# Performance work log

Hardware: AMD Instinct MI355X
Metric: run time of the kernel (lower is better)

## Reference

```python
import jax, jax.numpy as jnp
import numpy as np

B, N, K = 2, 8192, 16
D_IN, D_OUT = 32, 128
EPS = 1e-5


def _bn(x, gamma, beta):
    # x: (B, C, L); BatchNorm1d training-mode stats over (B, L)
    mean = x.mean(axis=(0, 2), keepdims=True)
    var = x.var(axis=(0, 2), keepdims=True)
    return gamma[None, :, None] * (x - mean) * jax.lax.rsqrt(var + EPS) + beta[None, :, None]


def _shared_mlp(x, w, b, gamma, beta, act):
    # SharedMLP: 1x1 Conv1d (channel GEMM) + BN + activation. x: (B, Cin, L)
    y = jnp.einsum('oi,bil->bol', w, x) + b[None, :, None]
    return act(_bn(y, gamma, beta))


def _attentive_pool(x, w, b):
    # x: (B, C, N, K); per-(b,n,k) Linear over C, softmax over K, weighted sum over K
    scores = jnp.einsum('oc,bcnk->bonk', w, x) + b[None, :, None, None]
    scores = jax.nn.softmax(scores, axis=-1)
    return jnp.sum(scores * x, axis=-1)  # (B, C, N)  (torch keeps K=1 dim; squeezed by SharedMLP reshape)


def _knn(coords, k):
    # brute-force squared-L2 KNN excluding self (faiss IndexFlatL2 semantics)
    sq = jnp.sum(coords * coords, axis=-1)  # (B, N)
    d2 = sq[:, :, None] + sq[:, None, :] - 2.0 * jnp.einsum('bid,bjd->bij', coords, coords)
    n = coords.shape[1]
    d2 = jnp.where(jnp.eye(n, dtype=bool)[None], jnp.inf, d2)
    neg, idx = jax.lax.top_k(-d2, k)  # ascending squared distance
    return idx, jnp.maximum(-neg, 0.0)


def _lse(coords, features, idx, dist, w, b, gamma, beta):
    # LocalSpatialEncoding: gather neighbor coords, build 10-ch relative features, MLP, concat
    Bq, Nq, Kq = idx.shape
    neighbor = jax.vmap(lambda c, i: c[i])(coords, idx)  # (B, N, K, 3)
    center = jnp.broadcast_to(coords[:, :, None, :], neighbor.shape)
    rel = center - neighbor
    spatial = jnp.concatenate([center, neighbor, rel, dist[..., None]], axis=-1)  # (B, N, K, 10)
    spatial = spatial.transpose(0, 3, 1, 2).reshape(Bq, 10, Nq * Kq)
    sf = _shared_mlp(spatial, w, b, gamma, beta, jax.nn.relu).reshape(Bq, -1, Nq, Kq)
    feat = jnp.broadcast_to(features[..., None], (Bq, features.shape[1], Nq, Kq))
    return jnp.concatenate([sf, feat], axis=1)


def _forward(coords, features,
             mlp1_w, mlp1_b, mlp1_g, mlp1_bt,
             lse1_w, lse1_b, lse1_g, lse1_bt,
             mlpp1_w, mlpp1_b, mlpp1_g, mlpp1_bt,
             lse2_w, lse2_b, lse2_g, lse2_bt,
             mlp2_w, mlp2_b, mlp2_g, mlp2_bt,
             res_w, res_b, res_g, res_bt,
             pool1_w, pool1_b, pool2_w, pool2_b):
    # faiss output is detached in torch (numpy round-trip) -> stop_gradient
    idx, dist = _knn(jax.lax.stop_gradient(coords), K)
    lrelu02 = lambda v: jnp.where(v >= 0, v, 0.2 * v)   # LeakyReLU(0.2)
    lrelu01 = lambda v: jnp.where(v >= 0, v, 0.01 * v)  # default LeakyReLU
    x = _shared_mlp(features, mlp1_w, mlp1_b, mlp1_g, mlp1_bt, lrelu02)      # (B, 64, N)
    x = _lse(coords, x, idx, dist, lse1_w, lse1_b, lse1_g, lse1_bt)          # (B, 128, N, K)
    x = _attentive_pool(x, pool1_w, pool1_b)                                  # (B, 128, N)
    x = _shared_mlp(x, mlpp1_w, mlpp1_b, mlpp1_g, mlpp1_bt, jax.nn.relu)     # (B, 32, N)
    x = _lse(coords, x, idx, dist, lse2_w, lse2_b, lse2_g, lse2_bt)          # (B, 64, N, K)
    x = _attentive_pool(x, pool2_w, pool2_b)                                  # (B, 64, N)
    x_main = _shared_mlp(x, mlp2_w, mlp2_b, mlp2_g, mlp2_bt, jax.nn.relu)    # (B, 128, N)
    resid = _shared_mlp(features, res_w, res_b, res_g, res_bt, jax.nn.relu)  # (B, 128, N)
    return lrelu01(jnp.concatenate([x_main, resid], axis=1))                 # (B, 256, N)


def setup_inputs() -> dict:
    key = jax.random.key(0)
    ks = iter(jax.random.split(key, 64))

    def lin(ci, co):
        w = jax.random.normal(next(ks), (co, ci), jnp.float32) / np.float32(np.sqrt(ci))
        b = jax.random.normal(next(ks), (co,), jnp.float32) * 0.01
        return w, b

    inp = {}
    inp['coords'] = jax.random.normal(next(ks), (B, N, 3), jnp.float32)
    inp['features'] = jax.random.normal(next(ks), (B, D_IN, N), jnp.float32)
    for name, ci, co in [('mlp1', D_IN, D_OUT // 2), ('lse1', 10, D_OUT // 2),
                         ('mlpp1', D_OUT, D_OUT // 4), ('lse2', 10, D_OUT // 4),
                         ('mlp2', D_OUT // 2, D_OUT), ('res', D_IN, D_OUT)]:
        w, b = lin(ci, co)
        inp[name + '_w'], inp[name + '_b'] = w, b
        inp[name + '_g'] = jnp.ones((co,), jnp.float32)
        inp[name + '_bt'] = jnp.zeros((co,), jnp.float32)
    for name, c in [('pool1', D_OUT), ('pool2', D_OUT // 2)]:
        w, b = lin(c, c)
        inp[name + '_w'], inp[name + '_b'] = w, b
    return inp


def reference(coords, features,
              mlp1_w, mlp1_b, mlp1_g, mlp1_bt,
              lse1_w, lse1_b, lse1_g, lse1_bt,
              mlpp1_w, mlpp1_b, mlpp1_g, mlpp1_bt,
              lse2_w, lse2_b, lse2_g, lse2_bt,
              mlp2_w, mlp2_b, mlp2_g, mlp2_bt,
              res_w, res_b, res_g, res_bt,
              pool1_w, pool1_b, pool2_w, pool2_b):
    return _forward(coords, features,
                    mlp1_w, mlp1_b, mlp1_g, mlp1_bt,
                    lse1_w, lse1_b, lse1_g, lse1_bt,
                    mlpp1_w, mlpp1_b, mlpp1_g, mlpp1_bt,
                    lse2_w, lse2_b, lse2_g, lse2_bt,
                    mlp2_w, mlp2_b, mlp2_g, mlp2_bt,
                    res_w, res_b, res_g, res_bt,
                    pool1_w, pool1_b, pool2_w, pool2_b)
```

## Files before the change

kernel.cpp:

```cpp
#include <hip/hip_runtime.h>

static constexpr int N_ = 8192;
static constexpr int B_ = 2;
static constexpr int K_ = 16;

typedef __attribute__((ext_vector_type(8))) short bf16x8;
typedef __attribute__((ext_vector_type(4))) float f32x4;

__device__ __forceinline__ short f2bf(float f) {
  unsigned int u = __float_as_uint(f);
  unsigned int r = (u + 0x7FFFu + ((u >> 16) & 1u)) >> 16;
  return (short)r;
}
__device__ __forceinline__ float bf2f(short h) {
  return __uint_as_float(((unsigned int)(unsigned short)h) << 16);
}

__global__ __launch_bounds__(512) void knn_kernel(const float* __restrict__ coords,
                                                  const int tbeg, const int tend,
                                                  float* __restrict__ skd, int* __restrict__ ski,
                                                  int* __restrict__ oidx, float* __restrict__ odist) {
  __shared__ float4 pts[2048];
  const int b = blockIdx.y;
  const int wv = threadIdx.x >> 6;
  const int lane = threadIdx.x & 63;
  const int q = blockIdx.x * 8 + wv;
  const float* cb = coords + (size_t)b * N_ * 3;
  const float qx = cb[q * 3 + 0], qy = cb[q * 3 + 1], qz = cb[q * 3 + 2];
  const float qsq = fmaf(qx, qx, fmaf(qy, qy, qz * qz));
  const int qblk = q & ~63;
  const unsigned long long qbit = ~(1ull << (q & 63));
  float kd = INFINITY;
  int ki = 0;
  if (tbeg > 0 && lane < 16) {
    kd = skd[((size_t)b * N_ + q) * K_ + lane];
    ki = ski[((size_t)b * N_ + q) * K_ + lane];
  }
  float tau = __shfl(kd, 15);
  for (int t0 = tbeg; t0 < tend; t0 += 2048) {
    __syncthreads();
    for (int i = threadIdx.x; i < 2048; i += 512) {
      const int p = t0 + i;
      const float x = cb[p * 3 + 0], y = cb[p * 3 + 1], z = cb[p * 3 + 2];
      pts[i] = make_float4(x, y, z, fmaf(x, x, fmaf(y, y, z * z)));
    }
    __syncthreads();
    for (int s = 0; s < 2048; s += 64) {
      const float4 p = pts[s + lane];
      const int base = t0 + s;
      const float dot = fmaf(qx, p.x, fmaf(qy, p.y, qz * p.z));
      const float d2 = fmaf(-2.0f, dot, qsq + p.w);
      unsigned long long m = __ballot(d2 < tau);
      if (base == qblk) m &= qbit;
      while (m) {
        const int src = __builtin_ctzll(m);
        const float dc = __shfl(d2, src);
        const int jc = base + src;
        const float sd = __shfl_up(kd, 1);
        const int si = __shfl_up(ki, 1);
        const bool c1 = kd > dc;
        const bool c2 = (lane > 0) && (sd > dc);
        kd = c1 ? (c2 ? sd : dc) : kd;
        ki = c1 ? (c2 ? si : jc) : ki;
        m &= (m - 1);
        tau = __shfl(kd, 15);
        m &= __ballot(d2 < tau);
      }
    }
  }
  if (lane < 16) {
    if (tend < N_) {
      skd[((size_t)b * N_ + q) * K_ + lane] = kd;
      ski[((size_t)b * N_ + q) * K_ + lane] = ki;
    } else {
      oidx[((size_t)b * N_ + q) * K_ + lane] = ki;
      odist[((size_t)b * N_ + q) * K_ + lane] = fmaxf(kd, 0.0f);
    }
  }
}

__device__ __forceinline__ float snn_get(const float* SNN, int a, int b) {
  const int i = a < b ? a : b, j = a < b ? b : a;
  return SNN[i == 0 ? j : (i == 1 ? 2 + j : 3 + j)];
}
__device__ __forceinline__ float mom_mean(int i, const float* C, const float* SN, float Sd) {
  if (i < 3) return 16.0f * C[i];
  if (i < 6) return SN[i - 3];
  if (i < 9) return 16.0f * C[i - 6] - SN[i - 6];
  return Sd;
}
__device__ __forceinline__ float mom_prod(int i, int j, const float* C, const float* SN,
                                          const float* SNN, float Sd, float Sdd, const float* SND) {
  const int ti = i < 3 ? 0 : (i < 6 ? 1 : (i < 9 ? 2 : 3));
  const int tj = j < 3 ? 0 : (j < 6 ? 1 : (j < 9 ? 2 : 3));
  const int a = (ti == 3) ? 0 : (i - ti * 3);
  const int bb = (tj == 3) ? 0 : (j - tj * 3);
  if (ti == 0 && tj == 0) return 16.0f * C[a] * C[bb];
  if (ti == 0 && tj == 1) return C[a] * SN[bb];
  if (ti == 0 && tj == 2) return C[a] * (16.0f * C[bb] - SN[bb]);
  if (ti == 0 && tj == 3) return C[a] * Sd;
  if (ti == 1 && tj == 1) return snn_get(SNN, a, bb);
  if (ti == 1 && tj == 2) return C[bb] * SN[a] - snn_get(SNN, a, bb);
  if (ti == 1 && tj == 3) return SND[a];
  if (ti == 2 && tj == 2) return 16.0f * C[a] * C[bb] - C[a] * SN[bb] - C[bb] * SN[a] + snn_get(SNN, a, bb);
  if (ti == 2 && tj == 3) return C[a] * Sd - SND[a];
  return Sdd;
}

__global__ __launch_bounds__(256) void moments_kernel(const float* __restrict__ coords,
                                                      const int* __restrict__ knn_i,
                                                      const float* __restrict__ knn_d,
                                                      double* __restrict__ mom) {
  __shared__ float sh[16][65];
  const int k = threadIdx.x & 15;
  const int pl = threadIdx.x >> 4;
  float accv = 0.0f;
  for (int batch = 0; batch < 4; ++batch) {
    const int pt = (blockIdx.x * 4 + batch) * 16 + pl;
    const int b = pt >> 13, n = pt & (N_ - 1);
    const float* cb = coords + (size_t)b * N_ * 3;
    const float cx = cb[n * 3 + 0], cy = cb[n * 3 + 1], cz = cb[n * 3 + 2];
    const int id = knn_i[(size_t)pt * K_ + k];
    const float dd = knn_d[(size_t)pt * K_ + k];
    const float nx = cb[id * 3 + 0], ny = cb[id * 3 + 1], nz = cb[id * 3 + 2];
    float v[14] = {nx, ny, nz, nx * nx, nx * ny, nx * nz, ny * ny, ny * nz, nz * nz,
                   dd, dd * dd, nx * dd, ny * dd, nz * dd};
#pragma unroll
    for (int e = 0; e < 14; ++e) {
      v[e] += __shfl_xor(v[e], 1);
      v[e] += __shfl_xor(v[e], 2);
      v[e] += __shfl_xor(v[e], 4);
      v[e] += __shfl_xor(v[e], 8);
    }
    if (k == 0) {
      const float C[3] = {cx, cy, cz};
      const float SN[3] = {v[0], v[1], v[2]};
      const float SNN[6] = {v[3], v[4], v[5], v[6], v[7], v[8]};
      const float Sd = v[9], Sdd = v[10];
      const float SND[3] = {v[11], v[12], v[13]};
      float m65[65];
      int e = 0;
#pragma unroll
      for (int i = 0; i < 10; ++i) m65[e++] = mom_mean(i, C, SN, Sd);
#pragma unroll
      for (int i = 0; i < 10; ++i)
#pragma unroll
        for (int j = i; j < 10; ++j) m65[e++] = mom_prod(i, j, C, SN, SNN, Sd, Sdd, SND);
#pragma unroll
      for (int q2 = 0; q2 < 65; ++q2) sh[pl][q2] = m65[q2];
    }
    __syncthreads();
    if (threadIdx.x < 65) {
      float s = 0.0f;
#pragma unroll
      for (int r = 0; r < 16; ++r) s += sh[r][threadIdx.x];
      accv += s;
    }
    __syncthreads();
  }
  if (threadIdx.x < 65) atomicAdd(&mom[threadIdx.x], (double)accv);
}

template <int CI, int CO>
__device__ __forceinline__ void conv_frag_seg(const float* __restrict__ w, short* __restrict__ H,
                                              short* __restrict__ L, int tid, int nthr) {
  constexpr int NT = CO / 16;
  for (int i = tid; i < CI * CO; i += nthr) {
    const int j = i & 7, l = (i >> 3) & 63, tmp = i >> 9;
    const int tt = tmp % NT, cc = tmp / NT;
    const int c = cc * 32 + (l >> 4) * 8 + j;
    const int o = tt * 16 + (l & 15);
    const float v = w[o * CI + c];
    const short h = f2bf(v);
    H[i] = h;
    L[i] = f2bf(v - bf2f(h));
  }
}

__global__ __launch_bounds__(256) void convert_kernel(
    const float* __restrict__ pw1, const float* __restrict__ pw2,
    short* __restrict__ wB1, short* __restrict__ wB2,
    const float* __restrict__ wm1, short* __restrict__ f1H, short* __restrict__ f1L,
    const float* __restrict__ wmp, short* __restrict__ f2H, short* __restrict__ f2L,
    const float* __restrict__ wm2, short* __restrict__ f3H, short* __restrict__ f3L,
    const float* __restrict__ wrs, short* __restrict__ fRH, short* __restrict__ fRL) {
  const int blk = blockIdx.x;
  if (blk < 8) {
    const int tid = blk * 256 + threadIdx.x;
    for (int i = tid; i < 128 * 128; i += 2048) wB1[i] = f2bf(pw1[i]);
  } else if (blk < 10) {
    const int tid = (blk - 8) * 256 + threadIdx.x;
    for (int i = tid; i < 64 * 64; i += 512) wB2[i] = f2bf(pw2[i]);
  } else if (blk < 12) {
    conv_frag_seg<32, 64>(wm1, f1H, f1L, (blk - 10) * 256 + threadIdx.x, 512);
  } else if (blk < 16) {
    conv_frag_seg<128, 32>(wmp, f2H, f2L, (blk - 12) * 256 + threadIdx.x, 1024);
  } else if (blk < 24) {
    conv_frag_seg<64, 128>(wm2, f3H, f3L, (blk - 16) * 256 + threadIdx.x, 2048);
  } else {
    conv_frag_seg<32, 128>(wrs, fRH, fRL, (blk - 24) * 256 + threadIdx.x, 1024);
  }
}

__global__ void setup_kernel(const double* __restrict__ mom,
                             const float* __restrict__ w1, const float* __restrict__ b1,
                             const float* __restrict__ g1, const float* __restrict__ t1,
                             const float* __restrict__ w2, const float* __restrict__ b2,
                             const float* __restrict__ g2, const float* __restrict__ t2,
                             float* __restrict__ w1f8, float* __restrict__ w2f8) {
  const int t = threadIdx.x;
  __shared__ double mu[10];
  __shared__ double S[10][10];
  const double cnt = (double)B_ * N_ * K_;
  if (t < 10) mu[t] = mom[t] / cnt;
  if (t < 55) {
    int e = t, i = 0;
    while (e >= 10 - i) { e -= 10 - i; ++i; }
    const int j = i + e;
    const double v = mom[10 + t] / cnt;
    S[i][j] = v;
    S[j][i] = v;
  }
  __syncthreads();
  const float *w, *bias, *gg, *bt;
  float *wf;
  int c;
  if (t < 64) { w = w1; bias = b1; gg = g1; bt = t1; wf = w1f8; c = t; }
  else if (t < 96) { w = w2; bias = b2; gg = g2; bt = t2; wf = w2f8; c = t - 64; }
  else return;
  double wd[10];
#pragma unroll
  for (int d = 0; d < 10; ++d) wd[d] = (double)w[c * 10 + d];
  const double cbv = (double)bias[c];
  double mz = cbv;
  for (int d = 0; d < 10; ++d) mz += wd[d] * mu[d];
  double e2 = cbv * cbv;
  for (int d = 0; d < 10; ++d) e2 += 2.0 * cbv * wd[d] * mu[d];
  for (int d = 0; d < 10; ++d)
    for (int e = 0; e < 10; ++e) e2 += wd[d] * wd[e] * S[d][e];
  const double var = e2 - mz * mz;
  const double a = (double)gg[c] / sqrt(var + 1e-5);
  const double shift = (double)bt[c] - a * mz;
  wf[c * 8 + 0] = (float)(a * (wd[0] + wd[6]));
  wf[c * 8 + 1] = (float)(a * (wd[1] + wd[7]));
  wf[c * 8 + 2] = (float)(a * (wd[2] + wd[8]));
  wf[c * 8 + 3] = (float)(a * (wd[3] - wd[6]));
  wf[c * 8 + 4] = (float)(a * (wd[4] - wd[7]));
  wf[c * 8 + 5] = (float)(a * (wd[5] - wd[8]));
  wf[c * 8 + 6] = (float)(a * wd[9]);
  wf[c * 8 + 7] = (float)(a * cbv + shift);
}

template <int CI, int CO, bool ROWMAJ>
__global__ __launch_bounds__(256) void gemm_mfma_kernel(const float* __restrict__ in,
                                                        const short* __restrict__ fragH,
                                                        const short* __restrict__ fragL,
                                                        const float* __restrict__ bias,
                                                        float* __restrict__ out,
                                                        double* __restrict__ sacc) {
  constexpr int NT = CO / 16;
  constexpr int NC = CI / 32;
  __shared__ float part[4][CO][2];
  const int wv = threadIdx.x >> 6, l = threadIdx.x & 63;
  const int col = l & 15, quad = l >> 4;
  const int p0 = blockIdx.x * 64 + wv * 16;
  const int pt = p0 + col;
  f32x4 d[NT];
#pragma unroll
  for (int t = 0; t < NT; ++t) {
    const float bv = bias[t * 16 + col];
    d[t][0] = bv; d[t][1] = bv; d[t][2] = bv; d[t][3] = bv;
  }
#pragma unroll
  for (int cc = 0; cc < NC; ++cc) {
    float xv[8];
    if (ROWMAJ) {
      const float* ip = in + (size_t)pt * CI + cc * 32 + quad * 8;
      *(float4*)&xv[0] = *(const float4*)ip;
      *(float4*)&xv[4] = *(const float4*)(ip + 4);
    } else {
      const int b = pt >> 13, n = pt & (N_ - 1);
      const float* ip = in + ((size_t)b * CI + cc * 32 + quad * 8) * N_ + n;
#pragma unroll
      for (int j = 0; j < 8; ++j) xv[j] = ip[(size_t)j * N_];
    }
    union { bf16x8 v; short u[8]; } AH, AL;
#pragma unroll
    for (int j = 0; j < 8; ++j) {
      const short h = f2bf(xv[j]);
      AH.u[j] = h;
      AL.u[j] = f2bf(xv[j] - bf2f(h));
    }
#pragma unroll
    for (int t = 0; t < NT; ++t) {
      const size_t fo = ((size_t)(cc * NT + t) * 64 + l) * 8;
      const bf16x8 BH = *(const bf16x8*)(fragH + fo);
      const bf16x8 BL = *(const bf16x8*)(fragL + fo);
      d[t] = __builtin_amdgcn_mfma_f32_16x16x32_bf16(AH.v, BH, d[t], 0, 0, 0);
      d[t] = __builtin_amdgcn_mfma_f32_16x16x32_bf16(AH.v, BL, d[t], 0, 0, 0);
      d[t] = __builtin_amdgcn_mfma_f32_16x16x32_bf16(AL.v, BH, d[t], 0, 0, 0);
    }
  }
#pragma unroll
  for (int t = 0; t < NT; ++t) {
#pragma unroll
    for (int r = 0; r < 4; ++r)
      out[(size_t)(p0 + quad * 4 + r) * CO + t * 16 + col] = d[t][r];
    float s1 = d[t][0] + d[t][1] + d[t][2] + d[t][3];
    float s2 = d[t][0] * d[t][0] + d[t][1] * d[t][1] + d[t][2] * d[t][2] + d[t][3] * d[t][3];
    s1 += __shfl_xor(s1, 16); s1 += __shfl_xor(s1, 32);
    s2 += __shfl_xor(s2, 16); s2 += __shfl_xor(s2, 32);
    if (quad == 0) { part[wv][t * 16 + col][0] = s1; part[wv][t * 16 + col][1] = s2; }
  }
  __syncthreads();
  if (threadIdx.x < CO) {
    const int o = threadIdx.x;
    atomicAdd(&sacc[o], (double)(part[0][o][0] + part[1][o][0] + part[2][o][0] + part[3][o][0]));
    atomicAdd(&sacc[CO + o], (double)(part[0][o][1] + part[1][o][1] + part[2][o][1] + part[3][o][1]));
  }
}

template <int CSF, int CF>
__global__ __launch_bounds__(256) void pool_kernel(
    const float* __restrict__ coords, const int* __restrict__ knn_i, const float* __restrict__ knn_d,
    const float* __restrict__ w8,
    const float* __restrict__ feat, const double* __restrict__ sfe,
    const float* __restrict__ gfe, const float* __restrict__ tfe,
    const float slope,
    const short* __restrict__ wB, const float* __restrict__ pb,
    float* __restrict__ out) {
  constexpr int C = CSF + CF;
  constexpr int CP = C + 4;
  constexpr int NT = C / 16;
  constexpr int NC = C / 32;
  __shared__ float xcat[4][16][CP];
  __shared__ float4 sp4[4][16];
  __shared__ float4 spc[4];
  const int g = threadIdx.x >> 6;
  const int l = threadIdx.x & 63;
  const int quad = l >> 4, col = l & 15;
  const int pid = blockIdx.x * 4 + g;
  const int b = pid >> 13, n = pid & (N_ - 1);
  const float* cb = coords + (size_t)b * N_ * 3;

  if (l < 16) {
    const int id = knn_i[(size_t)pid * K_ + l];
    const float dd = knn_d[(size_t)pid * K_ + l];
    const float nx = cb[id * 3 + 0], ny = cb[id * 3 + 1], nz = cb[id * 3 + 2];
    sp4[g][l] = make_float4(nx, ny, nz, dd);
    if (l == 0) spc[g] = make_float4(cb[n * 3 + 0], cb[n * 3 + 1], cb[n * 3 + 2], 0.0f);
  }
  if (l < CF) {
    const double cnt = (double)(B_ * N_);
    const double mean = sfe[l] / cnt;
    const double var = sfe[CF + l] / cnt - mean * mean;
    const double av = (double)gfe[l] / sqrt(var + 1e-5);
    const float af = (float)av;
    const float bfv = (float)((double)tfe[l] - av * mean);
    float v = feat[(size_t)pid * CF + l];
    v = af * v + bfv;
    v = (v >= 0.0f) ? v : slope * v;
#pragma unroll
    for (int j = 0; j < 16; ++j) xcat[g][j][CSF + l] = v;
  }
  __syncthreads();
  if (l < CSF) {
    const float4 wA = *(const float4*)(w8 + l * 8);
    const float4 wBv = *(const float4*)(w8 + l * 8 + 4);
    const float4 C4 = spc[g];
    const float tterm = wBv.w + wA.x * C4.x + wA.y * C4.y + wA.z * C4.z;
#pragma unroll
    for (int k = 0; k < 16; ++k) {
      const float4 nk = sp4[g][k];
      const float z = tterm + wA.w * nk.x + wBv.x * nk.y + wBv.y * nk.z + wBv.z * nk.w;
      xcat[g][k][l] = fmaxf(z, 0.0f);
    }
  }
  __syncthreads();
  f32x4 d[NT];
#pragma unroll
  for (int t = 0; t < NT; ++t) {
    const float pbv = pb[t * 16 + col];
    d[t][0] = pbv; d[t][1] = pbv; d[t][2] = pbv; d[t][3] = pbv;
  }
#pragma unroll
  for (int cc = 0; cc < NC; ++cc) {
    const float* xr = &xcat[g][col][cc * 32 + quad * 8];
    const float4 xa = *(const float4*)xr;
    const float4 xb = *(const float4*)(xr + 4);
    union { bf16x8 v; short u[8]; } A;
    A.u[0] = f2bf(xa.x); A.u[1] = f2bf(xa.y); A.u[2] = f2bf(xa.z); A.u[3] = f2bf(xa.w);
    A.u[4] = f2bf(xb.x); A.u[5] = f2bf(xb.y); A.u[6] = f2bf(xb.z); A.u[7] = f2bf(xb.w);
#pragma unroll
    for (int t = 0; t < NT; ++t) {
      const bf16x8 Bv = *(const bf16x8*)(wB + (size_t)(t * 16 + col) * C + cc * 32 + quad * 8);
      d[t] = __builtin_amdgcn_mfma_f32_16x16x32_bf16(A.v, Bv, d[t], 0, 0, 0);
    }
  }
#pragma unroll
  for (int t = 0; t < NT; ++t) {
    float mx = fmaxf(fmaxf(d[t][0], d[t][1]), fmaxf(d[t][2], d[t][3]));
    mx = fmaxf(mx, __shfl_xor(mx, 16));
    mx = fmaxf(mx, __shfl_xor(mx, 32));
    float e0 = __expf(d[t][0] - mx), e1 = __expf(d[t][1] - mx);
    float e2 = __expf(d[t][2] - mx), e3 = __expf(d[t][3] - mx);
    float s = e0 + e1 + e2 + e3;
    s += __shfl_xor(s, 16);
    s += __shfl_xor(s, 32);
    const int o = t * 16 + col;
    float part = e0 * xcat[g][quad * 4 + 0][o] + e1 * xcat[g][quad * 4 + 1][o] +
                 e2 * xcat[g][quad * 4 + 2][o] + e3 * xcat[g][quad * 4 + 3][o];
    part += __shfl_xor(part, 16);
    part += __shfl_xor(part, 32);
    if (quad == 0) out[(size_t)pid * C + o] = part / s;
  }
}

__global__ __launch_bounds__(256) void final_kernel(const float* __restrict__ y3,
                                                    const float* __restrict__ yr,
                                                    const double* __restrict__ s3,
                                                    const float* __restrict__ g3, const float* __restrict__ t3,
                                                    const double* __restrict__ sr,
                                                    const float* __restrict__ gr, const float* __restrict__ tr,
                                                    float* __restrict__ out) {
  __shared__ float tile[256 * 17];
  const int blk = blockIdx.x;
  const int b = blk >> 9;
  const int n0 = (blk & 511) << 4;
  const int c = threadIdx.x;
  const float* src;
  const double* sa;
  const float *gp, *tp;
  int cc;
  if (c < 128) { src = y3; sa = s3; gp = g3; tp = t3; cc = c; }
  else { src = yr; sa = sr; gp = gr; tp = tr; cc = c - 128; }
  const double cnt = (double)(B_ * N_);
  const double mean = sa[cc] / cnt;
  const double var = sa[128 + cc] / cnt - mean * mean;
  const double avd = (double)gp[cc] / sqrt(var + 1e-5);
  const float av = (float)avd;
  const float bv = (float)((double)tp[cc] - avd * mean);
#pragma unroll
  for (int nl = 0; nl < 16; ++nl) {
    const float x = av * src[((size_t)(b * N_ + n0 + nl)) * 128 + cc] + bv;
    tile[c * 17 + nl] = fmaxf(x, 0.0f);
  }
  __syncthreads();
  const int np = c & 15, grp = c >> 4;
#pragma unroll
  for (int j = 0; j < 16; ++j) {
    const int c2 = grp * 16 + j;
    out[((size_t)(b * 256 + c2)) * N_ + n0 + np] = tile[c2 * 17 + np];
  }
}

extern "C" void kernel_launch(void* const* d_in, const int* in_sizes, int n_in,
                              void* d_out, int out_size, void* d_ws, size_t ws_size,
                              hipStream_t stream) {
  (void)in_sizes; (void)n_in; (void)out_size; (void)ws_size;
  const float* coords   = (const float*)d_in[0];
  const float* features = (const float*)d_in[1];
  const float* mlp1_w = (const float*)d_in[2];
  const float* mlp1_b = (const float*)d_in[3];
  const float* mlp1_g = (const float*)d_in[4];
  const float* mlp1_t = (const float*)d_in[5];
  const float* lse1_w = (const float*)d_in[6];
  const float* lse1_b = (const float*)d_in[7];
  const float* lse1_g = (const float*)d_in[8];
  const float* lse1_t = (const float*)d_in[9];
  const float* mlpp1_w = (const float*)d_in[10];
  const float* mlpp1_b = (const float*)d_in[11];
  const float* mlpp1_g = (const float*)d_in[12];
  const float* mlpp1_t = (const float*)d_in[13];
  const float* lse2_w = (const float*)d_in[14];
  const float* lse2_b = (const float*)d_in[15];
  const float* lse2_g = (const float*)d_in[16];
  const float* lse2_t = (const float*)d_in[17];
  const float* mlp2_w = (const float*)d_in[18];
  const float* mlp2_b = (const float*)d_in[19];
  const float* mlp2_g = (const float*)d_in[20];
  const float* mlp2_t = (const float*)d_in[21];
  const float* res_w = (const float*)d_in[22];
  const float* res_b = (const float*)d_in[23];
  const float* res_g = (const float*)d_in[24];
  const float* res_t = (const float*)d_in[25];
  const float* pool1_w = (const float*)d_in[26];
  const float* pool1_b = (const float*)d_in[27];
  const float* pool2_w = (const float*)d_in[28];
  const float* pool2_b = (const float*)d_in[29];

  float* wsf = (float*)d_ws;
  int* knn_i = (int*)d_ws;
  float* knn_d = wsf + 262144;
  float* y1 = wsf + 524288;
  float* pooled1 = wsf + 1572864;
  float* y2 = wsf + 3670016;
  float* pooled2 = wsf + 4194304;
  float* y3 = wsf + 5242880;
  float* yr = wsf + 7340032;
  double* dacc = (double*)(wsf + 9437184);
  double* mom = dacc;
  double* sacc_mlp1 = dacc + 65;
  double* sacc_mlpp1 = dacc + 193;
  double* sacc_mlp2 = dacc + 257;
  double* sacc_res = dacc + 513;
  float* fpar = wsf + 9437184 + 1600;
  float* w1f8 = fpar;
  float* w2f8 = w1f8 + 512;
  short* wB1 = (short*)(w2f8 + 256);
  short* wB2 = wB1 + 16384;
  short* f1H = wB2 + 4096;
  short* f1L = f1H + 2048;
  short* f2H = f1L + 2048;
  short* f2L = f2H + 4096;
  short* f3H = f2L + 4096;
  short* f3L = f3H + 8192;
  short* fRH = f3L + 8192;
  short* fRL = fRH + 4096;
  float* skd = wsf + 9468224;
  int* ski = (int*)(skd + 262144);

  hipMemsetAsync(dacc, 0, 769 * sizeof(double), stream);
  knn_kernel<<<dim3(N_ / 8, B_), 512, 0, stream>>>(coords, 0, N_ / 2, skd, ski, knn_i, knn_d);
  knn_kernel<<<dim3(N_ / 8, B_), 512, 0, stream>>>(coords, N_ / 2, N_, skd, ski, knn_i, knn_d);
  convert_kernel<<<28, 256, 0, stream>>>(pool1_w, pool2_w, wB1, wB2,
                                         mlp1_w, f1H, f1L, mlpp1_w, f2H, f2L,
                                         mlp2_w, f3H, f3L, res_w, fRH, fRL);
  moments_kernel<<<256, 256, 0, stream>>>(coords, knn_i, knn_d, mom);
  setup_kernel<<<1, 128, 0, stream>>>(mom, lse1_w, lse1_b, lse1_g, lse1_t,
                                      lse2_w, lse2_b, lse2_g, lse2_t, w1f8, w2f8);
  gemm_mfma_kernel<32, 64, false><<<256, 256, 0, stream>>>(features, f1H, f1L, mlp1_b, y1, sacc_mlp1);
  pool_kernel<64, 64><<<B_ * N_ / 4, 256, 0, stream>>>(
      coords, knn_i, knn_d, w1f8, y1, sacc_mlp1, mlp1_g, mlp1_t, 0.2f, wB1, pool1_b, pooled1);
  gemm_mfma_kernel<128, 32, true><<<256, 256, 0, stream>>>(pooled1, f2H, f2L, mlpp1_b, y2, sacc_mlpp1);
  pool_kernel<32, 32><<<B_ * N_ / 4, 256, 0, stream>>>(
      coords, knn_i, knn_d, w2f8, y2, sacc_mlpp1, mlpp1_g, mlpp1_t, 0.0f, wB2, pool2_b, pooled2);
  gemm_mfma_kernel<64, 128, true><<<256, 256, 0, stream>>>(pooled2, f3H, f3L, mlp2_b, y3, sacc_mlp2);
  gemm_mfma_kernel<32, 128, false><<<256, 256, 0, stream>>>(features, fRH, fRL, res_b, yr, sacc_res);
  final_kernel<<<B_ * 512, 256, 0, stream>>>(y3, yr, sacc_mlp2, mlp2_g, mlp2_t,
                                             sacc_res, res_g, res_t, (float*)d_out);
}
```

Before: 414.9 us.

## Merge KNN passes and fuse prep, moments, setup and first GEMMs into fewer launches

The two-pass KNN (split target range with a scratch buffer carrying state between passes) becomes a single pass over all points, so the scratch round trip and one launch go away. The weight-conversion and moments kernels are merged into one prep_kernel. The setup kernel, the mlp1 GEMM and the residual GEMM are merged into one gemmA_kernel that picks its role from the block index. This cuts launch count and lets independent work share the GPU, but each KNN block now runs longer and the split may have been balancing occupancy.

```diff
diff --git a/kernel.cpp b/kernel.cpp
--- a/kernel.cpp
+++ b/kernel.cpp
@@ -17,9 +17,8 @@
 }
 
 __global__ __launch_bounds__(512) void knn_kernel(const float* __restrict__ coords,
-                                                  const int tbeg, const int tend,
-                                                  float* __restrict__ skd, int* __restrict__ ski,
-                                                  int* __restrict__ oidx, float* __restrict__ odist) {
+                                                  int* __restrict__ oidx,
+                                                  float* __restrict__ odist) {
   __shared__ float4 pts[2048];
   const int b = blockIdx.y;
   const int wv = threadIdx.x >> 6;
@@ -32,12 +31,8 @@
   const unsigned long long qbit = ~(1ull << (q & 63));
   float kd = INFINITY;
   int ki = 0;
-  if (tbeg > 0 && lane < 16) {
-    kd = skd[((size_t)b * N_ + q) * K_ + lane];
-    ki = ski[((size_t)b * N_ + q) * K_ + lane];
-  }
-  float tau = __shfl(kd, 15);
-  for (int t0 = tbeg; t0 < tend; t0 += 2048) {
+  float tau = INFINITY;
+  for (int t0 = 0; t0 < N_; t0 += 2048) {
     __syncthreads();
     for (int i = threadIdx.x; i < 2048; i += 512) {
       const int p = t0 + i;
@@ -69,13 +64,8 @@
     }
   }
   if (lane < 16) {
-    if (tend < N_) {
-      skd[((size_t)b * N_ + q) * K_ + lane] = kd;
-      ski[((size_t)b * N_ + q) * K_ + lane] = ki;
-    } else {
-      oidx[((size_t)b * N_ + q) * K_ + lane] = ki;
-      odist[((size_t)b * N_ + q) * K_ + lane] = fmaxf(kd, 0.0f);
-    }
+    oidx[((size_t)b * N_ + q) * K_ + lane] = ki;
+    odist[((size_t)b * N_ + q) * K_ + lane] = fmaxf(kd, 0.0f);
   }
 }
 
@@ -107,60 +97,6 @@
   return Sdd;
 }
 
-__global__ __launch_bounds__(256) void moments_kernel(const float* __restrict__ coords,
-                                                      const int* __restrict__ knn_i,
-                                                      const float* __restrict__ knn_d,
-                                                      double* __restrict__ mom) {
-  __shared__ float sh[16][65];
-  const int k = threadIdx.x & 15;
-  const int pl = threadIdx.x >> 4;
-  float accv = 0.0f;
-  for (int batch = 0; batch < 4; ++batch) {
-    const int pt = (blockIdx.x * 4 + batch) * 16 + pl;
-    const int b = pt >> 13, n = pt & (N_ - 1);
-    const float* cb = coords + (size_t)b * N_ * 3;
-    const float cx = cb[n * 3 + 0], cy = cb[n * 3 + 1], cz = cb[n * 3 + 2];
-    const int id = knn_i[(size_t)pt * K_ + k];
-    const float dd = knn_d[(size_t)pt * K_ + k];
-    const float nx = cb[id * 3 + 0], ny = cb[id * 3 + 1], nz = cb[id * 3 + 2];
-    float v[14] = {nx, ny, nz, nx * nx, nx * ny, nx * nz, ny * ny, ny * nz, nz * nz,
-                   dd, dd * dd, nx * dd, ny * dd, nz * dd};
-#pragma unroll
-    for (int e = 0; e < 14; ++e) {
-      v[e] += __shfl_xor(v[e], 1);
-      v[e] += __shfl_xor(v[e], 2);
-      v[e] += __shfl_xor(v[e], 4);
-      v[e] += __shfl_xor(v[e], 8);
-    }
-    if (k == 0) {
-      const float C[3] = {cx, cy, cz};
-      const float SN[3] = {v[0], v[1], v[2]};
-      const float SNN[6] = {v[3], v[4], v[5], v[6], v[7], v[8]};
-      const float Sd = v[9], Sdd = v[10];
-      const float SND[3] = {v[11], v[12], v[13]};
-      float m65[65];
-      int e = 0;
-#pragma unroll
-      for (int i = 0; i < 10; ++i) m65[e++] = mom_mean(i, C, SN, Sd);
-#pragma unroll
-      for (int i = 0; i < 10; ++i)
-#pragma unroll
-        for (int j = i; j < 10; ++j) m65[e++] = mom_prod(i, j, C, SN, SNN, Sd, Sdd, SND);
-#pragma unroll
-      for (int q2 = 0; q2 < 65; ++q2) sh[pl][q2] = m65[q2];
-    }
-    __syncthreads();
-    if (threadIdx.x < 65) {
-      float s = 0.0f;
-#pragma unroll
-      for (int r = 0; r < 16; ++r) s += sh[r][threadIdx.x];
-      accv += s;
-    }
-    __syncthreads();
-  }
-  if (threadIdx.x < 65) atomicAdd(&mom[threadIdx.x], (double)accv);
-}
-
 template <int CI, int CO>
 __device__ __forceinline__ void conv_frag_seg(const float* __restrict__ w, short* __restrict__ H,
                                               short* __restrict__ L, int tid, int nthr) {
@@ -177,40 +113,188 @@
   }
 }
 
-__global__ __launch_bounds__(256) void convert_kernel(
+__global__ __launch_bounds__(256) void prep_kernel(
     const float* __restrict__ pw1, const float* __restrict__ pw2,
     short* __restrict__ wB1, short* __restrict__ wB2,
     const float* __restrict__ wm1, short* __restrict__ f1H, short* __restrict__ f1L,
     const float* __restrict__ wmp, short* __restrict__ f2H, short* __restrict__ f2L,
     const float* __restrict__ wm2, short* __restrict__ f3H, short* __restrict__ f3L,
-    const float* __restrict__ wrs, short* __restrict__ fRH, short* __restrict__ fRL) {
+    const float* __restrict__ wrs, short* __restrict__ fRH, short* __restrict__ fRL,
+    const float* __restrict__ coords, const int* __restrict__ knn_i,
+    const float* __restrict__ knn_d, double* __restrict__ mom) {
   const int blk = blockIdx.x;
-  if (blk < 8) {
-    const int tid = blk * 256 + threadIdx.x;
-    for (int i = tid; i < 128 * 128; i += 2048) wB1[i] = f2bf(pw1[i]);
-  } else if (blk < 10) {
-    const int tid = (blk - 8) * 256 + threadIdx.x;
-    for (int i = tid; i < 64 * 64; i += 512) wB2[i] = f2bf(pw2[i]);
-  } else if (blk < 12) {
-    conv_frag_seg<32, 64>(wm1, f1H, f1L, (blk - 10) * 256 + threadIdx.x, 512);
-  } else if (blk < 16) {
-    conv_frag_seg<128, 32>(wmp, f2H, f2L, (blk - 12) * 256 + threadIdx.x, 1024);
-  } else if (blk < 24) {
-    conv_frag_seg<64, 128>(wm2, f3H, f3L, (blk - 16) * 256 + threadIdx.x, 2048);
-  } else {
-    conv_frag_seg<32, 128>(wrs, fRH, fRL, (blk - 24) * 256 + threadIdx.x, 1024);
-  }
-}
-
-__global__ void setup_kernel(const double* __restrict__ mom,
-                             const float* __restrict__ w1, const float* __restrict__ b1,
-                             const float* __restrict__ g1, const float* __restrict__ t1,
-                             const float* __restrict__ w2, const float* __restrict__ b2,
-                             const float* __restrict__ g2, const float* __restrict__ t2,
-                             float* __restrict__ w1f8, float* __restrict__ w2f8) {
+  if (blk < 11) {
+    if (blk < 4) {
+      for (int i = blk * 256 + threadIdx.x; i < 128 * 128; i += 1024) wB1[i] = f2bf(pw1[i]);
+    } else if (blk == 4) {
+      for (int i = threadIdx.x; i < 64 * 64; i += 256) wB2[i] = f2bf(pw2[i]);
+    } else if (blk == 5) {
+      conv_frag_seg<32, 64>(wm1, f1H, f1L, threadIdx.x, 256);
+    } else if (blk == 6) {
+      conv_frag_seg<128, 32>(wmp, f2H, f2L, threadIdx.x, 256);
+    } else if (blk < 9) {
+      conv_frag_seg<64, 128>(wm2, f3H, f3L, (blk - 7) * 256 + threadIdx.x, 512);
+    } else {
+      conv_frag_seg<32, 128>(wrs, fRH, fRL, (blk - 9) * 256 + threadIdx.x, 512);
+    }
+    return;
+  }
+  __shared__ float sh[16][65];
+  const int mb = blk - 11;
+  const int k = threadIdx.x & 15;
+  const int pl = threadIdx.x >> 4;
+  float accv = 0.0f;
+  for (int batch = 0; batch < 4; ++batch) {
+    const int pt = (mb * 4 + batch) * 16 + pl;
+    const int b = pt >> 13, n = pt & (N_ - 1);
+    const float* cb = coords + (size_t)b * N_ * 3;
+    const float cx = cb[n * 3 + 0], cy = cb[n * 3 + 1], cz = cb[n * 3 + 2];
+    const int id = knn_i[(size_t)pt * K_ + k];
+    const float dd = knn_d[(size_t)pt * K_ + k];
+    const float nx = cb[id * 3 + 0], ny = cb[id * 3 + 1], nz = cb[id * 3 + 2];
+    float v[14] = {nx, ny, nz, nx * nx, nx * ny, nx * nz, ny * ny, ny * nz, nz * nz,
+                   dd, dd * dd, nx * dd, ny * dd, nz * dd};
+#pragma unroll
+    for (int e = 0; e < 14; ++e) {
+      v[e] += __shfl_xor(v[e], 1);
+      v[e] += __shfl_xor(v[e], 2);
+      v[e] += __shfl_xor(v[e], 4);
+      v[e] += __shfl_xor(v[e], 8);
+    }
+    if (k == 0) {
+      const float C[3] = {cx, cy, cz};
+      const float SN[3] = {v[0], v[1], v[2]};
+      const float SNN[6] = {v[3], v[4], v[5], v[6], v[7], v[8]};
+      const float Sd = v[9], Sdd = v[10];
+      const float SND[3] = {v[11], v[12], v[13]};
+      float m65[65];
+      int e = 0;
+#pragma unroll
+      for (int i = 0; i < 10; ++i) m65[e++] = mom_mean(i, C, SN, Sd);
+#pragma unroll
+      for (int i = 0; i < 10; ++i)
+#pragma unroll
+        for (int j = i; j < 10; ++j) m65[e++] = mom_prod(i, j, C, SN, SNN, Sd, Sdd, SND);
+#pragma unroll
+      for (int q2 = 0; q2 < 65; ++q2) sh[pl][q2] = m65[q2];
+    }
+    __syncthreads();
+    if (threadIdx.x < 65) {
+      float s = 0.0f;
+#pragma unroll
+      for (int r = 0; r < 16; ++r) s += sh[r][threadIdx.x];
+      accv += s;
+    }
+    __syncthreads();
+  }
+  if (threadIdx.x < 65) atomicAdd(&mom[threadIdx.x], (double)accv);
+}
+
+template <int CI, int CO, bool ROWMAJ>
+__device__ __forceinline__ void gemm_body(const float* __restrict__ in,
+                                          const short* __restrict__ fragH,
+                                          const short* __restrict__ fragL,
+                                          const float* __restrict__ bias,
+                                          float* __restrict__ out,
+                                          double* __restrict__ sacc,
+                                          int blk, void* smem) {
+  constexpr int NT = CO / 16;
+  constexpr int NC = CI / 32;
+  float (*part)[CO][2] = (float (*)[CO][2])smem;
+  const int wv = threadIdx.x >> 6, l = threadIdx.x & 63;
+  const int col = l & 15, quad = l >> 4;
+  const int p0 = blk * 64 + wv * 16;
+  const int pt = p0 + col;
+  f32x4 d[NT];
+#pragma unroll
+  for (int t = 0; t < NT; ++t) {
+    const float bv = bias[t * 16 + col];
+    d[t][0] = bv; d[t][1] = bv; d[t][2] = bv; d[t][3] = bv;
+  }
+#pragma unroll
+  for (int cc = 0; cc < NC; ++cc) {
+    float xv[8];
+    if (ROWMAJ) {
+      const float* ip = in + (size_t)pt * CI + cc * 32 + quad * 8;
+      *(float4*)&xv[0] = *(const float4*)ip;
+      *(float4*)&xv[4] = *(const float4*)(ip + 4);
+    } else {
+      const int b = pt >> 13, n = pt & (N_ - 1);
+      const float* ip = in + ((size_t)b * CI + cc * 32 + quad * 8) * N_ + n;
+#pragma unroll
+      for (int j = 0; j < 8; ++j) xv[j] = ip[(size_t)j * N_];
+    }
+    union { bf16x8 v; short u[8]; } AH, AL;
+#pragma unroll
+    for (int j = 0; j < 8; ++j) {
+      const short h = f2bf(xv[j]);
+      AH.u[j] = h;
+      AL.u[j] = f2bf(xv[j] - bf2f(h));
+    }
+#pragma unroll
+    for (int t = 0; t < NT; ++t) {
+      const size_t fo = ((size_t)(cc * NT + t) * 64 + l) * 8;
+      const bf16x8 BH = *(const bf16x8*)(fragH + fo);
+      const bf16x8 BL = *(const bf16x8*)(fragL + fo);
+      d[t] = __builtin_amdgcn_mfma_f32_16x16x32_bf16(AH.v, BH, d[t], 0, 0, 0);
+      d[t] = __builtin_amdgcn_mfma_f32_16x16x32_bf16(AH.v, BL, d[t], 0, 0, 0);
+      d[t] = __builtin_amdgcn_mfma_f32_16x16x32_bf16(AL.v, BH, d[t], 0, 0, 0);
+    }
+  }
+#pragma unroll
+  for (int t = 0; t < NT; ++t) {
+#pragma unroll
+    for (int r = 0; r < 4; ++r)
+      out[(size_t)(p0 + quad * 4 + r) * CO + t * 16 + col] = d[t][r];
+    float s1 = d[t][0] + d[t][1] + d[t][2] + d[t][3];
+    float s2 = d[t][0] * d[t][0] + d[t][1] * d[t][1] + d[t][2] * d[t][2] + d[t][3] * d[t][3];
+    s1 += __shfl_xor(s1, 16); s1 += __shfl_xor(s1, 32);
+    s2 += __shfl_xor(s2, 16); s2 += __shfl_xor(s2, 32);
+    if (quad == 0) { part[wv][t * 16 + col][0] = s1; part[wv][t * 16 + col][1] = s2; }
+  }
+  __syncthreads();
+  if (threadIdx.x < CO) {
+    const int o = threadIdx.x;
+    atomicAdd(&sacc[o], (double)(part[0][o][0] + part[1][o][0] + part[2][o][0] + part[3][o][0]));
+    atomicAdd(&sacc[CO + o], (double)(part[0][o][1] + part[1][o][1] + part[2][o][1] + part[3][o][1]));
+  }
+}
+
+template <int CI, int CO, bool ROWMAJ>
+__global__ __launch_bounds__(256) void gemm_mfma_kernel(const float* __restrict__ in,
+                                                        const short* __restrict__ fragH,
+                                                        const short* __restrict__ fragL,
+                                                        const float* __restrict__ bias,
+                                                        float* __restrict__ out,
+                                                        double* __restrict__ sacc) {
+  __shared__ float part[4][CO][2];
+  gemm_body<CI, CO, ROWMAJ>(in, fragH, fragL, bias, out, sacc, blockIdx.x, (void*)part);
+}
+
+__global__ __launch_bounds__(256) void gemmA_kernel(
+    const float* __restrict__ features,
+    const short* __restrict__ f1H, const short* __restrict__ f1L,
+    const float* __restrict__ mlp1_b, float* __restrict__ y1, double* __restrict__ sacc1,
+    const short* __restrict__ fRH, const short* __restrict__ fRL,
+    const float* __restrict__ res_b, float* __restrict__ yr, double* __restrict__ saccR,
+    const double* __restrict__ mom,
+    const float* __restrict__ w1, const float* __restrict__ b1,
+    const float* __restrict__ g1, const float* __restrict__ t1,
+    const float* __restrict__ w2, const float* __restrict__ b2,
+    const float* __restrict__ g2, const float* __restrict__ t2,
+    float* __restrict__ w1f8, float* __restrict__ w2f8) {
+  __shared__ float part[4][128][2];
+  if (blockIdx.x < 256) {
+    gemm_body<32, 64, false>(features, f1H, f1L, mlp1_b, y1, sacc1, blockIdx.x, (void*)part);
+    return;
+  }
+  if (blockIdx.x < 512) {
+    gemm_body<32, 128, false>(features, fRH, fRL, res_b, yr, saccR, blockIdx.x - 256, (void*)part);
+    return;
+  }
   const int t = threadIdx.x;
-  __shared__ double mu[10];
-  __shared__ double S[10][10];
+  double* mu = (double*)part;
+  double* S = mu + 10;
   const double cnt = (double)B_ * N_ * K_;
   if (t < 10) mu[t] = mom[t] / cnt;
   if (t < 55) {
@@ -218,8 +302,8 @@
     while (e >= 10 - i) { e -= 10 - i; ++i; }
     const int j = i + e;
     const double v = mom[10 + t] / cnt;
-    S[i][j] = v;
-    S[j][i] = v;
+    S[i * 10 + j] = v;
+    S[j * 10 + i] = v;
   }
   __syncthreads();
   const float *w, *bias, *gg, *bt;
@@ -237,7 +321,7 @@
   double e2 = cbv * cbv;
   for (int d = 0; d < 10; ++d) e2 += 2.0 * cbv * wd[d] * mu[d];
   for (int d = 0; d < 10; ++d)
-    for (int e = 0; e < 10; ++e) e2 += wd[d] * wd[e] * S[d][e];
+    for (int e = 0; e < 10; ++e) e2 += wd[d] * wd[e] * S[d * 10 + e];
   const double var = e2 - mz * mz;
   const double a = (double)gg[c] / sqrt(var + 1e-5);
   const double shift = (double)bt[c] - a * mz;
@@ -249,75 +333,6 @@
   wf[c * 8 + 5] = (float)(a * (wd[5] - wd[8]));
   wf[c * 8 + 6] = (float)(a * wd[9]);
   wf[c * 8 + 7] = (float)(a * cbv + shift);
-}
-
-template <int CI, int CO, bool ROWMAJ>
-__global__ __launch_bounds__(256) void gemm_mfma_kernel(const float* __restrict__ in,
-                                                        const short* __restrict__ fragH,
-                                                        const short* __restrict__ fragL,
-                                                        const float* __restrict__ bias,
-                                                        float* __restrict__ out,
-                                                        double* __restrict__ sacc) {
-  constexpr int NT = CO / 16;
-  constexpr int NC = CI / 32;
-  __shared__ float part[4][CO][2];
-  const int wv = threadIdx.x >> 6, l = threadIdx.x & 63;
-  const int col = l & 15, quad = l >> 4;
-  const int p0 = blockIdx.x * 64 + wv * 16;
-  const int pt = p0 + col;
-  f32x4 d[NT];
-#pragma unroll
-  for (int t = 0; t < NT; ++t) {
-    const float bv = bias[t * 16 + col];
-    d[t][0] = bv; d[t][1] = bv; d[t][2] = bv; d[t][3] = bv;
-  }
-#pragma unroll
-  for (int cc = 0; cc < NC; ++cc) {
-    float xv[8];
-    if (ROWMAJ) {
-      const float* ip = in + (size_t)pt * CI + cc * 32 + quad * 8;
-      *(float4*)&xv[0] = *(const float4*)ip;
-      *(float4*)&xv[4] = *(const float4*)(ip + 4);
-    } else {
-      const int b = pt >> 13, n = pt & (N_ - 1);
-      const float* ip = in + ((size_t)b * CI + cc * 32 + quad * 8) * N_ + n;
-#pragma unroll
-      for (int j = 0; j < 8; ++j) xv[j] = ip[(size_t)j * N_];
-    }
-    union { bf16x8 v; short u[8]; } AH, AL;
-#pragma unroll
-    for (int j = 0; j < 8; ++j) {
-      const short h = f2bf(xv[j]);
-      AH.u[j] = h;
-      AL.u[j] = f2bf(xv[j] - bf2f(h));
-    }
-#pragma unroll
-    for (int t = 0; t < NT; ++t) {
-      const size_t fo = ((size_t)(cc * NT + t) * 64 + l) * 8;
-      const bf16x8 BH = *(const bf16x8*)(fragH + fo);
-      const bf16x8 BL = *(const bf16x8*)(fragL + fo);
-      d[t] = __builtin_amdgcn_mfma_f32_16x16x32_bf16(AH.v, BH, d[t], 0, 0, 0);
-      d[t] = __builtin_amdgcn_mfma_f32_16x16x32_bf16(AH.v, BL, d[t], 0, 0, 0);
-      d[t] = __builtin_amdgcn_mfma_f32_16x16x32_bf16(AL.v, BH, d[t], 0, 0, 0);
-    }
-  }
-#pragma unroll
-  for (int t = 0; t < NT; ++t) {
-#pragma unroll
-    for (int r = 0; r < 4; ++r)
-      out[(size_t)(p0 + quad * 4 + r) * CO + t * 16 + col] = d[t][r];
-    float s1 = d[t][0] + d[t][1] + d[t][2] + d[t][3];
-    float s2 = d[t][0] * d[t][0] + d[t][1] * d[t][1] + d[t][2] * d[t][2] + d[t][3] * d[t][3];
-    s1 += __shfl_xor(s1, 16); s1 += __shfl_xor(s1, 32);
-    s2 += __shfl_xor(s2, 16); s2 += __shfl_xor(s2, 32);
-    if (quad == 0) { part[wv][t * 16 + col][0] = s1; part[wv][t * 16 + col][1] = s2; }
-  }
-  __syncthreads();
-  if (threadIdx.x < CO) {
-    const int o = threadIdx.x;
-    atomicAdd(&sacc[o], (double)(part[0][o][0] + part[1][o][0] + part[2][o][0] + part[3][o][0]));
-    atomicAdd(&sacc[CO + o], (double)(part[0][o][1] + part[1][o][1] + part[2][o][1] + part[3][o][1]));
-  }
 }
 
 template <int CSF, int CF>
@@ -346,8 +361,7 @@
   if (l < 16) {
     const int id = knn_i[(size_t)pid * K_ + l];
     const float dd = knn_d[(size_t)pid * K_ + l];
-    const float nx = cb[id * 3 + 0], ny = cb[id * 3 + 1], nz = cb[id * 3 + 2];
-    sp4[g][l] = make_float4(nx, ny, nz, dd);
+    sp4[g][l] = make_float4(cb[id * 3 + 0], cb[id * 3 + 1], cb[id * 3 + 2], dd);
     if (l == 0) spc[g] = make_float4(cb[n * 3 + 0], cb[n * 3 + 1], cb[n * 3 + 2], 0.0f);
   }
   if (l < CF) {
@@ -517,26 +531,23 @@
   short* f3L = f3H + 8192;
   short* fRH = f3L + 8192;
   short* fRL = fRH + 4096;
-  float* skd = wsf + 9468224;
-  int* ski = (int*)(skd + 262144);
 
   hipMemsetAsync(dacc, 0, 769 * sizeof(double), stream);
-  knn_kernel<<<dim3(N_ / 8, B_), 512, 0, stream>>>(coords, 0, N_ / 2, skd, ski, knn_i, knn_d);
-  knn_kernel<<<dim3(N_ / 8, B_), 512, 0, stream>>>(coords, N_ / 2, N_, skd, ski, knn_i, knn_d);
-  convert_kernel<<<28, 256, 0, stream>>>(pool1_w, pool2_w, wB1, wB2,
-                                         mlp1_w, f1H, f1L, mlpp1_w, f2H, f2L,
-                                         mlp2_w, f3H, f3L, res_w, fRH, fRL);
-  moments_kernel<<<256, 256, 0, stream>>>(coords, knn_i, knn_d, mom);
-  setup_kernel<<<1, 128, 0, stream>>>(mom, lse1_w, lse1_b, lse1_g, lse1_t,
-                                      lse2_w, lse2_b, lse2_g, lse2_t, w1f8, w2f8);
-  gemm_mfma_kernel<32, 64, false><<<256, 256, 0, stream>>>(features, f1H, f1L, mlp1_b, y1, sacc_mlp1);
+  knn_kernel<<<dim3(N_ / 8, B_), 512, 0, stream>>>(coords, knn_i, knn_d);
+  prep_kernel<<<11 + 256, 256, 0, stream>>>(pool1_w, pool2_w, wB1, wB2,
+                                            mlp1_w, f1H, f1L, mlpp1_w, f2H, f2L,
+                                            mlp2_w, f3H, f3L, res_w, fRH, fRL,
+                                            coords, knn_i, knn_d, mom);
+  gemmA_kernel<<<513, 256, 0, stream>>>(features, f1H, f1L, mlp1_b, y1, sacc_mlp1,
+                                        fRH, fRL, res_b, yr, sacc_res, mom,
+                                        lse1_w, lse1_b, lse1_g, lse1_t,
+                                        lse2_w, lse2_b, lse2_g, lse2_t, w1f8, w2f8);
   pool_kernel<64, 64><<<B_ * N_ / 4, 256, 0, stream>>>(
       coords, knn_i, knn_d, w1f8, y1, sacc_mlp1, mlp1_g, mlp1_t, 0.2f, wB1, pool1_b, pooled1);
   gemm_mfma_kernel<128, 32, true><<<256, 256, 0, stream>>>(pooled1, f2H, f2L, mlpp1_b, y2, sacc_mlpp1);
   pool_kernel<32, 32><<<B_ * N_ / 4, 256, 0, stream>>>(
       coords, knn_i, knn_d, w2f8, y2, sacc_mlpp1, mlpp1_g, mlpp1_t, 0.0f, wB2, pool2_b, pooled2);
   gemm_mfma_kernel<64, 128, true><<<256, 256, 0, stream>>>(pooled2, f3H, f3L, mlp2_b, y3, sacc_mlp2);
-  gemm_mfma_kernel<32, 128, false><<<256, 256, 0, stream>>>(features, fRH, fRL, res_b, yr, sacc_res);
   final_kernel<<<B_ * 512, 256, 0, stream>>>(y3, yr, sacc_mlp2, mlp2_g, mlp2_t,
                                              sacc_res, res_g, res_t, (float*)d_out);
 }
```

After: 399.4 us. -3.7%, faster.
